# Optimization experiments

Measured on AMD Instinct MI355X. Metric: run time of the kernel, lower is better.

Reference implementation:

```python
import jax, jax.numpy as jnp
import numpy as np

NUM_HEADS = 8
STRIDE = 1
PAD = 1


def _conv(x, w, stride=STRIDE, pad=PAD):
    return jax.lax.conv_general_dilated(
        x, w, (stride, stride), [(pad, pad), (pad, pad)],
        dimension_numbers=("NCHW", "OIHW", "NCHW"))


def setup_inputs() -> dict:
    key = jax.random.key(0)
    ks = jax.random.split(key, 5)
    B, C, H, W = 8, 64, 56, 56
    nh = NUM_HEADS
    x = jax.random.normal(ks[0], (B, C, H, W), dtype=jnp.float32)
    # Conv weights, small init for numerical stability
    Wq = jax.random.normal(ks[1], (C * nh, C, 3, 3), dtype=jnp.float32) * 0.05
    Wk = jax.random.normal(ks[2], (C * nh, C, 3, 3), dtype=jnp.float32) * 0.05
    Wv = jax.random.normal(ks[3], (C * nh, C, 3, 3), dtype=jnp.float32) * 0.05
    Wu = jax.random.normal(ks[4], (C, C * nh, 1, 1), dtype=jnp.float32) * 0.05
    return {"x": x, "Wq": Wq, "Wk": Wk, "Wv": Wv, "Wu": Wu}


def reference(x, Wq, Wk, Wv, Wu):
    B, C, H, W = x.shape
    nh = NUM_HEADS
    # projections: [B, nh*C, H, W] -> [B, nh, C, H, W] -> [B, C, nh, H, W]
    def proj(w):
        y = _conv(x, w).reshape(B, nh, C, H, W)
        return jnp.transpose(y, (0, 2, 1, 3, 4))
    q = proj(Wq)  # [B, C, nh, H, W]
    k = proj(Wk)
    v = proj(Wv)
    scale = 1.0 / np.sqrt(C * nh).astype(np.float32)
    # contract over heads axis ('n'), attend over channel axis: [B, Cq, H, W, Ck]
    scores = jnp.einsum("bqnhw,bknhw->bqhwk", q, k) * scale
    attn = jax.nn.softmax(scores, axis=-1)
    # attended: [B, Cq, nh, H, W]
    attended = jnp.einsum("bqhwk,bknhw->bqnhw", attn, v)
    out = _conv(attended.reshape(B, C * nh, H, W), Wu, stride=1, pad=0)
    return jax.nn.relu(out)
```

## Files before the change

### kernel.cpp

```cpp
#include <hip/hip_runtime.h>
#include <hip/hip_bf16.h>

#define HW   56
#define CIN  64
#define OC   512
#define NPIX (HW * HW)
#define PEL  ((size_t)8 * NPIX * OC)

typedef unsigned short ushort_t;
typedef __attribute__((ext_vector_type(8))) short short8;
typedef __attribute__((ext_vector_type(4))) float floatx4;
typedef __attribute__((ext_vector_type(16))) float floatx16;

static __device__ __forceinline__ ushort_t f2bf(float f) {
  __hip_bfloat16 h = __float2bfloat16(f);
  return *(ushort_t*)&h;
}

#if __has_builtin(__builtin_amdgcn_exp2f)
#define EXP2F(x) __builtin_amdgcn_exp2f(x)
#else
#define EXP2F(x) exp2f(x)
#endif

__global__ __launch_bounds__(256)
void prep_kernel(const float* __restrict__ x, const float* __restrict__ W0,
                 const float* __restrict__ W1, const float* __restrict__ W2,
                 const float* __restrict__ Wu, ushort_t* __restrict__ xT,
                 ushort_t* __restrict__ Wb, ushort_t* __restrict__ WuP) {
  __shared__ ushort_t lx[CIN * HW];
  const int bid = blockIdx.x;
  const int tid = threadIdx.x;

  if (bid < 448) {
    const int h = bid % HW, b = bid / HW;
    for (int idx = tid; idx < CIN * HW; idx += 256) {
      int c = idx / HW, w = idx - c * HW;
      lx[idx] = f2bf(x[((size_t)(b * CIN + c) * HW + h) * HW + w]);
    }
    __syncthreads();
    ushort_t* dst = xT + ((size_t)(b * HW + h)) * HW * CIN;
    for (int i = tid; i < (CIN * HW) / 4; i += 256) {
      int e0 = i * 4;
      int w = e0 >> 6, c0 = e0 & 63;
      ushort4 o;
      o.x = lx[(c0 + 0) * HW + w];
      o.y = lx[(c0 + 1) * HW + w];
      o.z = lx[(c0 + 2) * HW + w];
      o.w = lx[(c0 + 3) * HW + w];
      ((ushort4*)dst)[i] = o;
    }
  } else if (bid < 832) {
    const int u = bid - 448;
    const int sel = u / 128;
    const int j = (u % 128) * 4 + (tid >> 6);
    const int cin = tid & 63;
    const float* W = sel == 0 ? W0 : (sel == 1 ? W1 : W2);
    ushort_t* Ds = Wb + (size_t)sel * 9 * OC * CIN;
    const int src = (sel < 2) ? ((j & 7) * 64 + (j >> 3)) : j;
    #pragma unroll
    for (int tap = 0; tap < 9; ++tap)
      Ds[((size_t)tap * OC + j) * CIN + cin] = f2bf(W[(size_t)src * 576 + cin * 9 + tap]);
  } else {
    const int el = (bid - 832) * 256 + tid;
    WuP[el] = f2bf(Wu[el]);
  }
}

#define XLS 72
#define XROW (58 * XLS)

__global__ __launch_bounds__(256, 2)
void conv3x3_qkv(const ushort_t* __restrict__ xT, const ushort_t* __restrict__ Wb,
                 ushort_t* __restrict__ yq) {
  __shared__ __align__(16) ushort_t xl[6 * XROW];

  const int tid  = threadIdx.x;
  const int lane = tid & 63;
  const int wv   = tid >> 6;
  const int g    = blockIdx.x;
  const int ob   = blockIdx.y;
  const int b    = blockIdx.z;
  const int h0   = g * 4;
  const int l31  = lane & 31;
  const int khi  = lane >> 5;

  int rowcol[7], rowv[7];
  #pragma unroll
  for (int t = 0; t < 7; ++t) {
    int p = t * 32 + l31;
    int row = p / HW, ww = p - row * HW;
    rowcol[t] = (row * 58 + ww) * XLS;
    rowv[t] = row;
  }

  const ushort_t* wb0 = Wb + ((size_t)(ob * 128 + wv * 32 + l31)) * CIN + khi * 8;

  for (int r = 0; r < 6; ++r) {
    int gh = h0 - 1 + r;
    const int sw = 2 * ((-r) & 3);
    if (gh >= 0 && gh < HW) {
      const uint4* src = (const uint4*)(xT + ((size_t)(b * HW + gh) * HW) * CIN);
      for (int idx = tid; idx < 448; idx += 256) {
        int w = idx >> 3, c8 = idx & 7;
        int col = 1 + w;
        int p8 = (c8 + sw) & 7;
        *(uint4*)&xl[(r * 58 + col) * XLS + p8 * 8] = src[idx];
      }
      if (tid < 16) {
        int col = (tid >> 3) ? 57 : 0, c8 = tid & 7;
        int p8 = (c8 + sw) & 7;
        *(uint4*)&xl[(r * 58 + col) * XLS + p8 * 8] = (uint4){0, 0, 0, 0};
      }
    } else {
      for (int idx = tid; idx < 464; idx += 256) {
        int col = idx >> 3, c8 = idx & 7;
        int p8 = (c8 + sw) & 7;
        *(uint4*)&xl[(r * 58 + col) * XLS + p8 * 8] = (uint4){0, 0, 0, 0};
      }
    }
  }

  short8 BfA[4], BfB[4];
  #pragma unroll
  for (int ck = 0; ck < 4; ++ck)
    BfA[ck] = *(const short8*)(wb0 + ck * 16);

  __syncthreads();

  #pragma unroll 1
  for (int s = 0; s < 3; ++s) {
    floatx16 acc[7];
    #pragma unroll
    for (int t = 0; t < 7; ++t) acc[t] = (floatx16)(0.0f);

    #pragma unroll
    for (int tap = 0; tap < 9; ++tap) {
      const int wtap = s * 9 + tap;
      if (wtap < 26) {
        #pragma unroll
        for (int ck = 0; ck < 4; ++ck)
          BfB[ck] = *(const short8*)(wb0 + (size_t)(wtap + 1) * (OC * CIN) + ck * 16);
      }
      const int kh = tap / 3, kw = tap - kh * 3;
      int baddr[7], b8[7];
      #pragma unroll
      for (int t = 0; t < 7; ++t) {
        baddr[t] = rowcol[t] + (kh * 58 + kw) * XLS;
        b8[t] = khi + 2 * ((-(rowv[t] + kh)) & 3);
      }
      __builtin_amdgcn_s_setprio(1);
      #pragma unroll
      for (int ck = 0; ck < 4; ++ck) {
        #pragma unroll
        for (int t = 0; t < 7; ++t) {
          int chunk = (b8[t] + 2 * ck) & 7;
          short8 af = *(const short8*)&xl[baddr[t] + chunk * 8];
          acc[t] = __builtin_amdgcn_mfma_f32_32x32x16_bf16(af, BfA[ck], acc[t], 0, 0, 0);
        }
      }
      __builtin_amdgcn_s_setprio(0);
      #pragma unroll
      for (int ck = 0; ck < 4; ++ck) BfA[ck] = BfB[ck];
    }

    ushort_t* y = yq + (size_t)s * PEL;
    const int oc = ob * 128 + wv * 32 + l31;
    #pragma unroll
    for (int t = 0; t < 7; ++t) {
      #pragma unroll
      for (int i = 0; i < 16; ++i) {
        int p = t * 32 + (i & 3) + 8 * (i >> 2) + 4 * khi;
        int row = p / HW, ww = p - row * HW;
        size_t pb = ((size_t)((b * HW + h0 + row) * HW + ww)) * OC;
        y[pb + oc] = f2bf(acc[t][i]);
      }
    }
  }
}

#define PST  72
#define A2ST 520

__global__ __launch_bounds__(256, 3)
void attn_kernel(const ushort_t* __restrict__ q, const ushort_t* __restrict__ k,
                 const ushort_t* __restrict__ v, const ushort_t* __restrict__ WuP,
                 float* __restrict__ out) {
  __shared__ __align__(16) ushort_t Pl[4][64 * PST];
  __shared__ __align__(16) ushort_t a2[16 * A2ST];

  const int tid  = threadIdx.x;
  const int lane = tid & 63;
  const int wv   = tid >> 6;
  const int l15  = lane & 15;
  const int quad = lane >> 4;
  const int p0   = blockIdx.x * 16;
  const int b    = blockIdx.y;
  const size_t ibase = ((size_t)b * NPIX + p0) * 512;

  ushort_t* Pw = &Pl[wv][0];
  const float scale2 = 0.063758723f;

  auto loadpix = [&](int plocal, short8 qf[4], short8 kf[4], short8 vf[2]) {
    const ushort_t* qp = q + ibase + (size_t)plocal * 512;
    const ushort_t* kp = k + ibase + (size_t)plocal * 512;
    const ushort_t* vp = v + ibase + (size_t)plocal * 512;
    #pragma unroll
    for (int nt = 0; nt < 4; ++nt)
      qf[nt] = *(const short8*)(qp + (nt * 16 + l15) * 8);
    #pragma unroll
    for (int mt = 0; mt < 4; ++mt) {
      kf[mt] = (short8){0, 0, 0, 0, 0, 0, 0, 0};
      if (quad == 0) kf[mt] = *(const short8*)(kp + (mt * 16 + l15) * 8);
    }
    #pragma unroll
    for (int ck = 0; ck < 2; ++ck)
      vf[ck] = *(const short8*)(vp + (l15 & 7) * 64 + ck * 32 + quad * 8);
  };

  short8 qf[4], kf[4], vf[2];
  loadpix(wv * 4, qf, kf, vf);

  #pragma unroll
  for (int i = 0; i < 4; ++i) {
    const int plocal = wv * 4 + i;
    short8 qn[4], kn[4], vn[2];
    if (i < 3) loadpix(plocal + 1, qn, kn, vn);

    floatx4 S[4][4];
    #pragma unroll
    for (int mt = 0; mt < 4; ++mt)
      #pragma unroll
      for (int nt = 0; nt < 4; ++nt) S[mt][nt] = (floatx4){0.f, 0.f, 0.f, 0.f};
    __builtin_amdgcn_s_setprio(1);
    #pragma unroll
    for (int mt = 0; mt < 4; ++mt)
      #pragma unroll
      for (int nt = 0; nt < 4; ++nt)
        S[mt][nt] = __builtin_amdgcn_mfma_f32_16x16x32_bf16(kf[mt], qf[nt], S[mt][nt], 0, 0, 0);
    __builtin_amdgcn_s_setprio(0);

    float inv[4];
    #pragma unroll
    for (int nt = 0; nt < 4; ++nt) {
      float e[4][4];
      #pragma unroll
      for (int mt = 0; mt < 4; ++mt)
        #pragma unroll
        for (int r = 0; r < 4; ++r)
          e[mt][r] = EXP2F(S[mt][nt][r] * scale2);
      float sm[4];
      #pragma unroll
      for (int mt = 0; mt < 4; ++mt)
        sm[mt] = (e[mt][0] + e[mt][1]) + (e[mt][2] + e[mt][3]);
      float sum = (sm[0] + sm[1]) + (sm[2] + sm[3]);
      sum += __shfl_xor(sum, 16);
      sum += __shfl_xor(sum, 32);
      inv[nt] = __builtin_amdgcn_rcpf(sum);
      #pragma unroll
      for (int mt = 0; mt < 4; ++mt) {
        ushort4 w4;
        w4.x = f2bf(e[mt][0]);
        w4.y = f2bf(e[mt][1]);
        w4.z = f2bf(e[mt][2]);
        w4.w = f2bf(e[mt][3]);
        *(ushort4*)&Pw[(nt * 16 + l15) * PST + mt * 16 + quad * 4] = w4;
      }
    }

    floatx4 T[4];
    #pragma unroll
    for (int nt = 0; nt < 4; ++nt) T[nt] = (floatx4){0.f, 0.f, 0.f, 0.f};
    __builtin_amdgcn_s_setprio(1);
    #pragma unroll
    for (int ck = 0; ck < 2; ++ck) {
      #pragma unroll
      for (int nt = 0; nt < 4; ++nt) {
        short8 pf = *(const short8*)&Pw[(nt * 16 + l15) * PST + ck * 32 + quad * 8];
        T[nt] = __builtin_amdgcn_mfma_f32_16x16x32_bf16(vf[ck], pf, T[nt], 0, 0, 0);
      }
    }
    __builtin_amdgcn_s_setprio(0);
    if (quad < 2) {
      #pragma unroll
      for (int nt = 0; nt < 4; ++nt) {
        ushort4 w4;
        w4.x = f2bf(T[nt][0] * inv[nt]);
        w4.y = f2bf(T[nt][1] * inv[nt]);
        w4.z = f2bf(T[nt][2] * inv[nt]);
        w4.w = f2bf(T[nt][3] * inv[nt]);
        *(ushort4*)&a2[plocal * A2ST + (nt * 16 + l15) * 8 + quad * 4] = w4;
      }
    }

    if (i < 3) {
      #pragma unroll
      for (int z = 0; z < 4; ++z) { qf[z] = qn[z]; kf[z] = kn[z]; }
      vf[0] = vn[0];
      vf[1] = vn[1];
    }
  }
  __syncthreads();

  floatx4 O = (floatx4){0.f, 0.f, 0.f, 0.f};
  #pragma unroll
  for (int ck = 0; ck < 16; ++ck) {
    short8 aw = *(const short8*)(WuP + (size_t)(wv * 16 + l15) * 512 + ck * 32 + quad * 8);
    short8 bw = *(const short8*)&a2[l15 * A2ST + ck * 32 + quad * 8];
    O = __builtin_amdgcn_mfma_f32_16x16x32_bf16(aw, bw, O, 0, 0, 0);
  }
  #pragma unroll
  for (int r = 0; r < 4; ++r) {
    int co = wv * 16 + quad * 4 + r;
    out[((size_t)b * 64 + co) * NPIX + p0 + l15] = fmaxf(O[r], 0.f);
  }
}

extern "C" void kernel_launch(void* const* d_in, const int* in_sizes, int n_in,
                              void* d_out, int out_size, void* d_ws, size_t ws_size,
                              hipStream_t stream) {
  const float* x  = (const float*)d_in[0];
  const float* Wq = (const float*)d_in[1];
  const float* Wk = (const float*)d_in[2];
  const float* Wv = (const float*)d_in[3];
  const float* Wu = (const float*)d_in[4];
  float* out = (float*)d_out;

  const size_t xT_elems = (size_t)8 * NPIX * CIN;
  const size_t w_elems  = (size_t)9 * OC * CIN;
  const size_t wu_elems = (size_t)64 * 512;
  ushort_t* xT  = (ushort_t*)d_ws;
  ushort_t* Wb  = xT + xT_elems;
  ushort_t* WuP = Wb + 3 * w_elems;
  ushort_t* q   = WuP + wu_elems;
  ushort_t* k   = q + PEL;
  ushort_t* v   = k + PEL;

  prep_kernel<<<960, 256, 0, stream>>>(x, Wq, Wk, Wv, Wu, xT, Wb, WuP);

  dim3 cgrid(14, 4, 8);
  conv3x3_qkv<<<cgrid, 256, 0, stream>>>(xT, Wb, q);

  attn_kernel<<<dim3(NPIX / 16, 8), 256, 0, stream>>>(q, k, v, WuP, out);
}
```

Baseline: 150.6 us.

## Fuse input transpose/bf16 conversion into conv load; stage weight prep through LDS

The separate pass that transposes x to NHWC bf16 in the workspace is removed. The conv kernel now reads fp32 NCHW x directly and converts it to bf16 while filling its shared-memory tile. Weight prep now stages each filter's 576 floats through LDS so the global reads are coalesced. This drops one write and one read of the intermediate buffer, but the conv tile loads become strided 4-byte gathers across channels (stride NPIX), and each x row is reloaded by every output-block and row-group CTA.

Measured after the change: 156.8 us. 1.04x slower.

```diff
diff --git a/kernel.cpp b/kernel.cpp
--- a/kernel.cpp
+++ b/kernel.cpp
@@ -24,45 +24,35 @@
 #endif
 
 __global__ __launch_bounds__(256)
-void prep_kernel(const float* __restrict__ x, const float* __restrict__ W0,
-                 const float* __restrict__ W1, const float* __restrict__ W2,
-                 const float* __restrict__ Wu, ushort_t* __restrict__ xT,
-                 ushort_t* __restrict__ Wb, ushort_t* __restrict__ WuP) {
-  __shared__ ushort_t lx[CIN * HW];
+void prep_w(const float* __restrict__ W0, const float* __restrict__ W1,
+            const float* __restrict__ W2, const float* __restrict__ Wu,
+            ushort_t* __restrict__ Wb, ushort_t* __restrict__ WuP) {
   const int bid = blockIdx.x;
   const int tid = threadIdx.x;
 
-  if (bid < 448) {
-    const int h = bid % HW, b = bid / HW;
-    for (int idx = tid; idx < CIN * HW; idx += 256) {
-      int c = idx / HW, w = idx - c * HW;
-      lx[idx] = f2bf(x[((size_t)(b * CIN + c) * HW + h) * HW + w]);
-    }
-    __syncthreads();
-    ushort_t* dst = xT + ((size_t)(b * HW + h)) * HW * CIN;
-    for (int i = tid; i < (CIN * HW) / 4; i += 256) {
-      int e0 = i * 4;
-      int w = e0 >> 6, c0 = e0 & 63;
-      ushort4 o;
-      o.x = lx[(c0 + 0) * HW + w];
-      o.y = lx[(c0 + 1) * HW + w];
-      o.z = lx[(c0 + 2) * HW + w];
-      o.w = lx[(c0 + 3) * HW + w];
-      ((ushort4*)dst)[i] = o;
-    }
-  } else if (bid < 832) {
-    const int u = bid - 448;
-    const int sel = u / 128;
-    const int j = (u % 128) * 4 + (tid >> 6);
-    const int cin = tid & 63;
+  if (bid < 384) {
+    __shared__ float lw[4 * 576];
+    const int sel = bid / 128;
+    const int jbase = (bid % 128) * 4;
     const float* W = sel == 0 ? W0 : (sel == 1 ? W1 : W2);
     ushort_t* Ds = Wb + (size_t)sel * 9 * OC * CIN;
-    const int src = (sel < 2) ? ((j & 7) * 64 + (j >> 3)) : j;
+
+    #pragma unroll
+    for (int q = 0; q < 4; ++q) {
+      const int j = jbase + q;
+      const int src = (sel < 2) ? ((j & 7) * 64 + (j >> 3)) : j;
+      for (int i = tid; i < 576; i += 256)
+        lw[q * 576 + i] = W[(size_t)src * 576 + i];
+    }
+    __syncthreads();
+
+    const int q = tid >> 6, cin = tid & 63;
+    const int j = jbase + q;
     #pragma unroll
     for (int tap = 0; tap < 9; ++tap)
-      Ds[((size_t)tap * OC + j) * CIN + cin] = f2bf(W[(size_t)src * 576 + cin * 9 + tap]);
+      Ds[((size_t)tap * OC + j) * CIN + cin] = f2bf(lw[q * 576 + cin * 9 + tap]);
   } else {
-    const int el = (bid - 832) * 256 + tid;
+    const int el = (bid - 384) * 256 + tid;
     WuP[el] = f2bf(Wu[el]);
   }
 }
@@ -71,7 +61,7 @@
 #define XROW (58 * XLS)
 
 __global__ __launch_bounds__(256, 2)
-void conv3x3_qkv(const ushort_t* __restrict__ xT, const ushort_t* __restrict__ Wb,
+void conv3x3_qkv(const float* __restrict__ x, const ushort_t* __restrict__ Wb,
                  ushort_t* __restrict__ yq) {
   __shared__ __align__(16) ushort_t xl[6 * XROW];
 
@@ -100,12 +90,17 @@
     int gh = h0 - 1 + r;
     const int sw = 2 * ((-r) & 3);
     if (gh >= 0 && gh < HW) {
-      const uint4* src = (const uint4*)(xT + ((size_t)(b * HW + gh) * HW) * CIN);
+      const float* src = x + ((size_t)(b * CIN) * HW + gh) * HW;
       for (int idx = tid; idx < 448; idx += 256) {
         int w = idx >> 3, c8 = idx & 7;
         int col = 1 + w;
         int p8 = (c8 + sw) & 7;
-        *(uint4*)&xl[(r * 58 + col) * XLS + p8 * 8] = src[idx];
+        const float* s0 = src + (size_t)(c8 * 8) * NPIX + w;
+        short8 v;
+        #pragma unroll
+        for (int j = 0; j < 8; ++j)
+          v[j] = (short)f2bf(s0[(size_t)j * NPIX]);
+        *(short8*)&xl[(r * 58 + col) * XLS + p8 * 8] = v;
       }
       if (tid < 16) {
         int col = (tid >> 3) ? 57 : 0, c8 = tid & 7;
@@ -326,20 +321,18 @@
   const float* Wu = (const float*)d_in[4];
   float* out = (float*)d_out;
 
-  const size_t xT_elems = (size_t)8 * NPIX * CIN;
   const size_t w_elems  = (size_t)9 * OC * CIN;
   const size_t wu_elems = (size_t)64 * 512;
-  ushort_t* xT  = (ushort_t*)d_ws;
-  ushort_t* Wb  = xT + xT_elems;
+  ushort_t* Wb  = (ushort_t*)d_ws;
   ushort_t* WuP = Wb + 3 * w_elems;
   ushort_t* q   = WuP + wu_elems;
   ushort_t* k   = q + PEL;
   ushort_t* v   = k + PEL;
 
-  prep_kernel<<<960, 256, 0, stream>>>(x, Wq, Wk, Wv, Wu, xT, Wb, WuP);
+  prep_w<<<512, 256, 0, stream>>>(Wq, Wk, Wv, Wu, Wb, WuP);
 
   dim3 cgrid(14, 4, 8);
-  conv3x3_qkv<<<cgrid, 256, 0, stream>>>(xT, Wb, q);
+  conv3x3_qkv<<<cgrid, 256, 0, stream>>>(x, Wb, q);
 
   attn_kernel<<<dim3(NPIX / 16, 8), 256, 0, stream>>>(q, k, v, WuP, out);
 }
```
